# Kernel optimization log

Hardware: AMD Instinct MI355X
Metric: run time of the kernel (lower is better)

## Reference

```python
import jax, jax.numpy as jnp
import numpy as np

RES = 16            # voxel grid resolution (init arg res)
G = RES ** 3        # number of cells = 4096
REG_R = float(np.sqrt(3.0)) / RES  # sqrt(3)/s regularizer radius
B, C, RND, NPTS, H = 16, 64, 2, 16384, 256


def _grid_offsets():
    # util.meshgrid(res): integer grid coords, then ((grid+0.5)/res - 0.5).view(3,-1)
    r = jnp.arange(RES)
    gx, gy, gz = jnp.meshgrid(r, r, r, indexing='ij')
    grid = jnp.stack([gx, gy, gz], 0).reshape(3, -1).astype(jnp.float32)  # [3, G]
    return (grid + 0.5) / RES - 0.5


def _dens_sample(dens, n_points):
    # Deterministic largest-remainder allocation of n_points proportional to density.
    b = dens.shape[0]
    p = dens.reshape(b, -1)
    p = p / jnp.sum(p, axis=-1, keepdims=True)
    scaled = p * n_points                      # [b, G]
    base = jnp.floor(scaled)
    rem = (n_points - jnp.sum(base, axis=-1)).astype(jnp.int32)   # [b]
    frac = scaled - base
    ranks = jnp.argsort(jnp.argsort(-frac, axis=-1), axis=-1)      # rank by fractional part
    return base.astype(jnp.int32) + (ranks < rem[:, None]).astype(jnp.int32)  # [b, G]


def setup_inputs() -> dict:
    key = jax.random.key(0)
    ks = jax.random.split(key, 9)
    cin = C + RND
    f32 = jnp.float32
    return {
        'x': jax.random.normal(ks[0], (B, C, RES, RES, RES), f32),
        'dens': jax.random.uniform(ks[1], (B, RES, RES, RES), f32) + 1e-3,
        'noise': jax.random.uniform(ks[2], (B, RND, NPTS), f32),
        'W1': jax.random.normal(ks[3], (H, cin), f32) * np.float32(1.0 / np.sqrt(cin)),
        'b1': jnp.zeros((H,), f32),
        'W2': jax.random.normal(ks[4], (H, H), f32) * np.float32(1.0 / np.sqrt(H)),
        'b2': jnp.zeros((H,), f32),
        'W3': jax.random.normal(ks[5], (3, H), f32) * np.float32(1.0 / np.sqrt(H)),
        'b3': jnp.zeros((3,), f32),
        'n_points': NPTS,
    }


def reference(x, dens, noise, W1, b1, W2, b2, W3, b3, n_points):
    b, c = x.shape[0], x.shape[1]
    x_flat = x.reshape(b, c, -1)                        # [b, c, G]
    n = _dens_sample(dens, n_points)                    # [b, G] repeat counts, sums to n_points
    # Vectorized replacement for the nonzero()/cat loop: cell i appears n[i] times.
    cell_ids = jnp.arange(G)
    idx = jax.vmap(lambda ni: jnp.repeat(cell_ids, ni, total_repeat_length=n_points))(n)  # [b, n_points]
    x_ind = jnp.take_along_axis(x_flat, idx[:, None, :], axis=2)   # [b, c, n_points]
    o = _grid_offsets()                                 # [3, G]
    gen_off = jnp.transpose(o[:, idx], (1, 0, 2))       # [b, 3, n_points]
    rnd = noise * 2.0 - 1.0                             # uniform in [-1, 1)
    gen_inp = jnp.concatenate([x_ind, rnd], axis=1)     # [b, c+rnd, n_points]
    # pointwise conv1d MLP generator
    h = jax.nn.relu(jnp.einsum('oc,bcn->bon', W1, gen_inp) + b1[:, None])
    h = jax.nn.relu(jnp.einsum('oh,bhn->bon', W2, h) + b2[:, None])
    out = jnp.einsum('oh,bhn->bon', W3, h) + b3[:, None]            # [b, 3, n_points]
    norm = jnp.sqrt(jnp.sum(out * out, axis=1))                      # [b, n_points]
    reg = jnp.maximum(norm - REG_R, 0.0)
    return (out + gen_off, reg)
```

## Files before the change

kernel.cpp:

```cpp
#include <hip/hip_runtime.h>

typedef unsigned long long u64;
typedef _Float16 f16x8 __attribute__((ext_vector_type(8)));
typedef float    f32x4 __attribute__((ext_vector_type(4)));
typedef __fp16   fp16x2 __attribute__((ext_vector_type(2)));

#define G_    4096
#define NPTS  16384

union H8 { _Float16 h[8]; uint4 u; };
union PK2 { fp16x2 h[2]; uint2 u; };
union PK4 { fp16x2 h[4]; uint4 u; };

#define MFMA_(A_,B_,C_) __builtin_amdgcn_mfma_f32_16x16x32_f16((A_),(B_),(C_),0,0,0)


#define OFF_W1F 1048576
#define OFF_W2F 1097728
#define OFF_W3F 1228800
#define OFF_XT  1236992
#define WS_NEED (OFF_XT + 8388608)

__global__ __launch_bounds__(256) void kP(const float* __restrict__ dens,
                                          int* __restrict__ pc,
                                          const float* __restrict__ W1,
                                          const float* __restrict__ W2,
                                          const float* __restrict__ W3,
                                          const float* __restrict__ x,
                                          _Float16* __restrict__ w1f,
                                          _Float16* __restrict__ w2f,
                                          _Float16* __restrict__ w3f,
                                          _Float16* __restrict__ xT){
  __shared__ double sred[256];
  __shared__ u64  keys[4096];
  __shared__ int  nvs[4096];
  __shared__ int  binidx[4096];
  __shared__ int  hist[1024];
  __shared__ int  cab[1024];
  __shared__ int  scan[256];
  __shared__ float Sf;
  __shared__ int  remS, BstarS, needS, cntS;
  const int t = threadIdx.x;

  if (blockIdx.x >= 62){
    const int idx = blockIdx.x - 62;
    const int b = idx >> 4, blk = idx & 15;
    const int cell = blk*256 + t;
    const float* xb = x + ((size_t)b*64)*G_ + cell;
    _Float16* xo = xT + ((size_t)(b*G_ + cell))*64;
    #pragma unroll
    for (int c8 = 0; c8 < 8; ++c8){
      float a[8];
      #pragma unroll
      for (int j = 0; j < 8; ++j) a[j] = xb[(size_t)(c8*8 + j)*G_];
      PK4 v;
      v.h[0] = __builtin_amdgcn_cvt_pkrtz(a[0], a[1]);
      v.h[1] = __builtin_amdgcn_cvt_pkrtz(a[2], a[3]);
      v.h[2] = __builtin_amdgcn_cvt_pkrtz(a[4], a[5]);
      v.h[3] = __builtin_amdgcn_cvt_pkrtz(a[6], a[7]);
      *(uint4*)&xo[c8*8] = v.u;
    }
    return;
  }

  if (blockIdx.x >= 16){
    const int e = (blockIdx.x - 16)*256 + t;
    H8 v;
    if (e < 8192){
      const int RT = e >> 9, kt = (e >> 6) & 7, l = e & 63;
      const int m = RT*16 + (l & 15), k = kt*32 + ((l >> 4) << 3);
      #pragma unroll
      for (int j = 0; j < 8; ++j) v.h[j] = (_Float16)W2[m*256 + k + j];
      *(uint4*)&w2f[e*8] = v.u;
    } else if (e < 11264){
      const int e2 = e - 8192;
      const int RT = e2 / 192, r2 = e2 % 192, kt = r2 >> 6, l = r2 & 63;
      const int m = RT*16 + (l & 15), k = kt*32 + ((l >> 4) << 3);
      #pragma unroll
      for (int j = 0; j < 8; ++j) v.h[j] = (k + j < 66) ? (_Float16)W1[m*66 + k + j] : (_Float16)0.f;
      *(uint4*)&w1f[e2*8] = v.u;
    } else if (e < 11776){
      const int e3 = e - 11264;
      const int kt = e3 >> 6, l = e3 & 63;
      const int m = l & 15, k = kt*32 + ((l >> 4) << 3);
      #pragma unroll
      for (int j = 0; j < 8; ++j) v.h[j] = (m < 3) ? (_Float16)W3[m*256 + k + j] : (_Float16)0.f;
      *(uint4*)&w3f[e3*8] = v.u;
    }
    return;
  }

  const int b = blockIdx.x;
  const float* d = dens + b*G_;

  for (int j = t; j < 1024; j += 256) hist[j] = 0;
  if (t == 0) cntS = 0;

  double s = 0.0;
  for (int j = 0; j < 16; ++j) s += (double)d[t + 256*j];
  sred[t] = s; __syncthreads();
  for (int off = 128; off > 0; off >>= 1){
    if (t < off) sred[t] += sred[t + off];
    __syncthreads();
  }
  if (t == 0) Sf = (float)sred[0];
  __syncthreads();
  const float S = Sf;

  int bi[16]; int bs = 0;
  #pragma unroll
  for (int j = 0; j < 16; ++j){
    const int i = t + 256*j;
    const float p  = d[i] / S;
    const float sc = p * 16384.0f;
    const float fl = floorf(sc);
    const float fr = sc - fl;
    bi[j] = (int)fl; bs += bi[j];
    const unsigned fb = __float_as_uint(fr);
    keys[i] = ((u64)fb << 12) | (u64)(4095 - i);
    atomicAdd(&hist[fb >> 20], 1);
  }
  scan[t] = bs; __syncthreads();
  for (int off = 128; off > 0; off >>= 1){
    if (t < off) scan[t] += scan[t + off];
    __syncthreads();
  }
  if (t == 0) remS = 16384 - scan[0];
  __syncthreads();
  const int rem = remS;

  const int h0 = hist[4*t], h1 = hist[4*t+1], h2 = hist[4*t+2], h3 = hist[4*t+3];
  const int gs = h0 + h1 + h2 + h3;
  __syncthreads();
  scan[t] = gs; __syncthreads();
  for (int off = 1; off < 256; off <<= 1){
    const int v2 = (t + off < 256) ? scan[t + off] : 0;
    __syncthreads();
    scan[t] += v2;
    __syncthreads();
  }
  const int sAfter = scan[t] - gs;
  cab[4*t+3] = sAfter;
  cab[4*t+2] = sAfter + h3;
  cab[4*t+1] = sAfter + h3 + h2;
  cab[4*t+0] = sAfter + h3 + h2 + h1;
  if (t == 0){ BstarS = 0x7fffffff; needS = 0; }
  __syncthreads();
  if (rem > 0){
    const int ca[4] = {cab[4*t], cab[4*t+1], cab[4*t+2], cab[4*t+3]};
    const int hh[4] = {h0, h1, h2, h3};
    #pragma unroll
    for (int q = 0; q < 4; ++q)
      if (ca[q] < rem && rem <= ca[q] + hh[q]){ BstarS = 4*t + q; needS = rem - ca[q]; }
  }
  __syncthreads();
  const int Bstar = BstarS, need = needS;

  #pragma unroll
  for (int j = 0; j < 16; ++j){
    const int i = t + 256*j;
    const int bin = (int)(keys[i] >> 32);
    nvs[i] = bi[j] + ((bin > Bstar) ? 1 : 0);
    if (bin == Bstar){ const int pos = atomicAdd(&cntS, 1); binidx[pos] = i; }
  }
  __syncthreads();
  const int cnt = cntS;
  for (int p = t; p < cnt; p += 256){
    const u64 K = keys[binidx[p]];
    int r = 0;
    for (int q = 0; q < cnt; ++q) r += (keys[binidx[q]] > K) ? 1 : 0;
    if (r < need) nvs[binidx[p]] += 1;
  }
  __syncthreads();

  int loc[16]; int ls = 0;
  #pragma unroll
  for (int j = 0; j < 16; ++j){ loc[j] = nvs[t*16 + j]; ls += loc[j]; }
  __syncthreads();
  scan[t] = ls; __syncthreads();
  for (int off = 1; off < 256; off <<= 1){
    const int v2 = (t >= off) ? scan[t - off] : 0;
    __syncthreads();
    scan[t] += v2;
    __syncthreads();
  }
  int off0 = scan[t] - ls;
  int* o = pc + b*NPTS;
  #pragma unroll
  for (int j = 0; j < 16; ++j){
    const int c = t*16 + j;
    for (int r = 0; r < loc[j]; ++r) o[off0++] = c;
  }
}

template<bool USE_XT>
__global__ __launch_bounds__(256, 3) void kE(
    const float* __restrict__ x, const _Float16* __restrict__ xT,
    const float* __restrict__ noise,
    const _Float16* __restrict__ w1f, const _Float16* __restrict__ w2f,
    const _Float16* __restrict__ w3f,
    const float* __restrict__ b1, const float* __restrict__ b2, const float* __restrict__ b3,
    const int* __restrict__ pc, float* __restrict__ out)
{
  __shared__ _Float16 Hb[16384];
  __shared__ int cells[64];
  const int b = blockIdx.y, p0 = blockIdx.x*64, tid = threadIdx.x;
  const int w = tid >> 6, lane = tid & 63;

  if (tid < 64) cells[tid] = pc[b*NPTS + p0 + tid];

  {
    const int ct = tid >> 6, l2 = tid & 63;
    const int k2 = l2 >> 4, pt = ct*16 + (l2 & 15);
    PK4 v; v.u = make_uint4(0u, 0u, 0u, 0u);
    if (k2 == 0){
      const float n0 = noise[(b*2 + 0)*NPTS + p0 + pt]*2.f - 1.f;
      const float n1 = noise[(b*2 + 1)*NPTS + p0 + pt]*2.f - 1.f;
      v.h[0] = __builtin_amdgcn_cvt_pkrtz(n0, n1);
    }
    *(uint4*)&Hb[((2*4 + ct)*64 + l2)*8] = v.u;
  }

  #pragma unroll
  for (int i = 0; i < 2; ++i){
    const int e = tid + 256*i;
    const int pt = e >> 3, koct = e & 7;
    const int cell = pc[b*NPTS + p0 + pt];
    const int kt = koct >> 2, k2 = koct & 3;
    const int lane2 = (pt & 15) + k2*16, ct = pt >> 4;
    if (USE_XT){
      const uint4 v = *(const uint4*)&xT[((size_t)(b*G_ + cell))*64 + koct*8];
      *(uint4*)&Hb[((kt*4 + ct)*64 + lane2)*8] = v;
    } else {
      const float* xb = x + ((size_t)(b*64 + koct*8))*G_ + cell;
      float a[8];
      #pragma unroll
      for (int j = 0; j < 8; ++j) a[j] = xb[(size_t)j*G_];
      PK4 v;
      v.h[0] = __builtin_amdgcn_cvt_pkrtz(a[0], a[1]);
      v.h[1] = __builtin_amdgcn_cvt_pkrtz(a[2], a[3]);
      v.h[2] = __builtin_amdgcn_cvt_pkrtz(a[4], a[5]);
      v.h[3] = __builtin_amdgcn_cvt_pkrtz(a[6], a[7]);
      *(uint4*)&Hb[((kt*4 + ct)*64 + lane2)*8] = v.u;
    }
  }
  __syncthreads();

  f32x4 acc[4][4];
  const f32x4 zz = {0.f, 0.f, 0.f, 0.f};
  #pragma unroll
  for (int rt = 0; rt < 4; ++rt)
    #pragma unroll
    for (int ct = 0; ct < 4; ++ct) acc[rt][ct] = zz;

  const int wr = w*4;

  __builtin_amdgcn_s_setprio(1);
  #pragma unroll
  for (int kt = 0; kt < 3; ++kt){
    f16x8 B[4];
    #pragma unroll
    for (int ct = 0; ct < 4; ++ct) B[ct] = *(f16x8*)&Hb[((kt*4 + ct)*64 + lane)*8];
    #pragma unroll
    for (int rt = 0; rt < 4; ++rt){
      f16x8 A = *(const f16x8*)&w1f[(((wr + rt)*3 + kt)*64 + lane)*8];
      #pragma unroll
      for (int ct = 0; ct < 4; ++ct)
        acc[rt][ct] = MFMA_(A, B[ct], acc[rt][ct]);
    }
  }
  __builtin_amdgcn_s_setprio(0);
  __syncthreads();

  #pragma unroll
  for (int rt = 0; rt < 4; ++rt){
    const int row0 = w*64 + rt*16 + ((lane >> 4) << 2);
    const float4 bq = *(const float4*)&b1[row0];
    const int kt2 = row0 >> 5, c16 = (row0 >> 3) & 3, j0 = row0 & 7;
    const int lane2 = (lane & 15) + c16*16;
    #pragma unroll
    for (int ct = 0; ct < 4; ++ct){
      PK2 v;
      v.h[0] = __builtin_amdgcn_cvt_pkrtz(fmaxf(acc[rt][ct][0] + bq.x, 0.f),
                                          fmaxf(acc[rt][ct][1] + bq.y, 0.f));
      v.h[1] = __builtin_amdgcn_cvt_pkrtz(fmaxf(acc[rt][ct][2] + bq.z, 0.f),
                                          fmaxf(acc[rt][ct][3] + bq.w, 0.f));
      *(uint2*)&Hb[((kt2*4 + ct)*64 + lane2)*8 + j0] = v.u;
      acc[rt][ct] = zz;
    }
  }
  __syncthreads();

  __builtin_amdgcn_s_setprio(1);
  #pragma unroll 4
  for (int kt = 0; kt < 8; ++kt){
    f16x8 B[4];
    #pragma unroll
    for (int ct = 0; ct < 4; ++ct) B[ct] = *(f16x8*)&Hb[((kt*4 + ct)*64 + lane)*8];
    #pragma unroll
    for (int rt = 0; rt < 4; ++rt){
      f16x8 A = *(const f16x8*)&w2f[(((wr + rt)*8 + kt)*64 + lane)*8];
      #pragma unroll
      for (int ct = 0; ct < 4; ++ct)
        acc[rt][ct] = MFMA_(A, B[ct], acc[rt][ct]);
    }
  }
  __builtin_amdgcn_s_setprio(0);

  f16x8 W3v[8];
  #pragma unroll
  for (int kt = 0; kt < 8; ++kt) W3v[kt] = *(const f16x8*)&w3f[(kt*64 + lane)*8];
  __syncthreads();

  #pragma unroll
  for (int rt = 0; rt < 4; ++rt){
    const int row0 = w*64 + rt*16 + ((lane >> 4) << 2);
    const float4 bq = *(const float4*)&b2[row0];
    const int kt2 = row0 >> 5, c16 = (row0 >> 3) & 3, j0 = row0 & 7;
    const int lane2 = (lane & 15) + c16*16;
    #pragma unroll
    for (int ct = 0; ct < 4; ++ct){
      PK2 v;
      v.h[0] = __builtin_amdgcn_cvt_pkrtz(fmaxf(acc[rt][ct][0] + bq.x, 0.f),
                                          fmaxf(acc[rt][ct][1] + bq.y, 0.f));
      v.h[1] = __builtin_amdgcn_cvt_pkrtz(fmaxf(acc[rt][ct][2] + bq.z, 0.f),
                                          fmaxf(acc[rt][ct][3] + bq.w, 0.f));
      *(uint2*)&Hb[((kt2*4 + ct)*64 + lane2)*8 + j0] = v.u;
    }
  }
  __syncthreads();

  f32x4 a3 = zz;
  __builtin_amdgcn_s_setprio(1);
  #pragma unroll
  for (int kt = 0; kt < 8; ++kt){
    f16x8 B = *(f16x8*)&Hb[((kt*4 + w)*64 + lane)*8];
    a3 = MFMA_(W3v[kt], B, a3);
  }
  __builtin_amdgcn_s_setprio(0);
  if (lane < 16){
    const float ox = a3[0] + b3[0];
    const float oy = a3[1] + b3[1];
    const float oz = a3[2] + b3[2];
    const float nrm = sqrtf(ox*ox + oy*oy + oz*oz);
    const float rg_ = fmaxf(nrm - (float)0.10825317547305482, 0.f);
    const int pt = w*16 + lane;
    const int cell = cells[pt];
    const float fx = ((float)(cell >> 8)        + 0.5f) * 0.0625f - 0.5f;
    const float fy = ((float)((cell >> 4) & 15) + 0.5f) * 0.0625f - 0.5f;
    const float fz = ((float)(cell & 15)        + 0.5f) * 0.0625f - 0.5f;
    const int pidx = p0 + pt;
    out[b*49152 +          pidx] = ox + fx;
    out[b*49152 + 16384 +  pidx] = oy + fy;
    out[b*49152 + 32768 +  pidx] = oz + fz;
    out[786432  + b*16384 + pidx] = rg_;
  }
}

extern "C" void kernel_launch(void* const* d_in, const int* in_sizes, int n_in,
                              void* d_out, int out_size, void* d_ws, size_t ws_size,
                              hipStream_t stream){
  const float* x     = (const float*)d_in[0];
  const float* dens  = (const float*)d_in[1];
  const float* noise = (const float*)d_in[2];
  const float* W1    = (const float*)d_in[3];
  const float* b1    = (const float*)d_in[4];
  const float* W2    = (const float*)d_in[5];
  const float* b2    = (const float*)d_in[6];
  const float* W3    = (const float*)d_in[7];
  const float* b3    = (const float*)d_in[8];

  char* ws = (char*)d_ws;
  int*      pc   = (int*)(ws + 0);
  _Float16* w1f  = (_Float16*)(ws + OFF_W1F);
  _Float16* w2f  = (_Float16*)(ws + OFF_W2F);
  _Float16* w3f  = (_Float16*)(ws + OFF_W3F);
  _Float16* xT   = (_Float16*)(ws + OFF_XT);
  float*    out  = (float*)d_out;

  const bool use_xt = (ws_size >= (size_t)WS_NEED);
  const int  nprep  = use_xt ? 318 : 62;

  kP<<<dim3(nprep), dim3(256), 0, stream>>>(dens, pc, W1, W2, W3, x,
                                            w1f, w2f, w3f, xT);
  if (use_xt)
    kE<true ><<<dim3(256, 16), dim3(256), 0, stream>>>(x, xT, noise, w1f, w2f, w3f,
                                                       b1, b2, b3, pc, out);
  else
    kE<false><<<dim3(256, 16), dim3(256), 0, stream>>>(x, xT, noise, w1f, w2f, w3f,
                                                       b1, b2, b3, pc, out);
}
```

Baseline: 84.17 us.

## Make MLP kernel persistent over four point tiles with prefetched gather

Each block now processes four consecutive 64-point tiles in a loop instead of one, launching a quarter as many blocks. The next tile's cell indices, noise and gathered x features are loaded into registers during the current tile's layer-1 and layer-2 MFMA work, then written to a separate input LDS buffer. This hides gather latency behind compute and amortizes block setup, at the cost of fewer blocks (1024) for latency hiding and more LDS and register use.

```diff
diff --git a/kernel.cpp b/kernel.cpp
--- a/kernel.cpp
+++ b/kernel.cpp
@@ -11,6 +11,7 @@
 union H8 { _Float16 h[8]; uint4 u; };
 union PK2 { fp16x2 h[2]; uint2 u; };
 union PK4 { fp16x2 h[4]; uint4 u; };
+union PK1 { fp16x2 h; unsigned u; };
 
 #define MFMA_(A_,B_,C_) __builtin_amdgcn_mfma_f32_16x16x32_f16((A_),(B_),(C_),0,0,0)
 
@@ -202,158 +203,206 @@
     const float* __restrict__ b1, const float* __restrict__ b2, const float* __restrict__ b3,
     const int* __restrict__ pc, float* __restrict__ out)
 {
-  __shared__ _Float16 Hb[16384];
-  __shared__ int cells[64];
-  const int b = blockIdx.y, p0 = blockIdx.x*64, tid = threadIdx.x;
+  __shared__ _Float16 Hin[6144];
+  __shared__ _Float16 Bh[16384];
+  const int b = blockIdx.y, tid = threadIdx.x;
   const int w = tid >> 6, lane = tid & 63;
-
-  if (tid < 64) cells[tid] = pc[b*NPTS + p0 + tid];
-
+  const int base0 = b*NPTS + blockIdx.x*256;
+
+  const int ptA = tid >> 3, koct = tid & 7;
+  const int ptB = ptA + 32;
+  const int ktS = koct >> 2, k2 = koct & 3;
+  const int hinA = (((ktS*4 + (ptA >> 4))*64) + (ptA & 15) + k2*16)*8;
+  const int hinB = (((ktS*4 + (ptB >> 4))*64) + (ptB & 15) + k2*16)*8;
+  const int l2 = tid & 63;
+  const int npt = (tid >> 6)*16 + (tid & 15);
+  const int hinN = ((2*4 + (tid >> 6))*64 + l2)*8;
+
+  const f32x4 zz = {0.f, 0.f, 0.f, 0.f};
+  const int wr = w*4;
+
+  *(uint4*)&Hin[((2*4 + (tid >> 6))*64 + l2)*8] = make_uint4(0u,0u,0u,0u);
   {
-    const int ct = tid >> 6, l2 = tid & 63;
-    const int k2 = l2 >> 4, pt = ct*16 + (l2 & 15);
-    PK4 v; v.u = make_uint4(0u, 0u, 0u, 0u);
-    if (k2 == 0){
-      const float n0 = noise[(b*2 + 0)*NPTS + p0 + pt]*2.f - 1.f;
-      const float n1 = noise[(b*2 + 1)*NPTS + p0 + pt]*2.f - 1.f;
-      v.h[0] = __builtin_amdgcn_cvt_pkrtz(n0, n1);
-    }
-    *(uint4*)&Hb[((2*4 + ct)*64 + l2)*8] = v.u;
-  }
-
-  #pragma unroll
-  for (int i = 0; i < 2; ++i){
-    const int e = tid + 256*i;
-    const int pt = e >> 3, koct = e & 7;
-    const int cell = pc[b*NPTS + p0 + pt];
-    const int kt = koct >> 2, k2 = koct & 3;
-    const int lane2 = (pt & 15) + k2*16, ct = pt >> 4;
+    const int cA = pc[base0 + ptA];
+    const int cB = pc[base0 + ptB];
+    float n0 = 0.f, n1 = 0.f;
+    if (l2 < 16){
+      n0 = noise[(b*2 + 0)*NPTS + blockIdx.x*256 + npt]*2.f - 1.f;
+      n1 = noise[(b*2 + 1)*NPTS + blockIdx.x*256 + npt]*2.f - 1.f;
+    }
+    uint4 sA, sB;
     if (USE_XT){
-      const uint4 v = *(const uint4*)&xT[((size_t)(b*G_ + cell))*64 + koct*8];
-      *(uint4*)&Hb[((kt*4 + ct)*64 + lane2)*8] = v;
+      sA = *(const uint4*)&xT[((size_t)(b*G_ + cA))*64 + koct*8];
+      sB = *(const uint4*)&xT[((size_t)(b*G_ + cB))*64 + koct*8];
     } else {
-      const float* xb = x + ((size_t)(b*64 + koct*8))*G_ + cell;
-      float a[8];
-      #pragma unroll
-      for (int j = 0; j < 8; ++j) a[j] = xb[(size_t)j*G_];
-      PK4 v;
-      v.h[0] = __builtin_amdgcn_cvt_pkrtz(a[0], a[1]);
-      v.h[1] = __builtin_amdgcn_cvt_pkrtz(a[2], a[3]);
-      v.h[2] = __builtin_amdgcn_cvt_pkrtz(a[4], a[5]);
-      v.h[3] = __builtin_amdgcn_cvt_pkrtz(a[6], a[7]);
-      *(uint4*)&Hb[((kt*4 + ct)*64 + lane2)*8] = v.u;
-    }
-  }
-  __syncthreads();
-
-  f32x4 acc[4][4];
-  const f32x4 zz = {0.f, 0.f, 0.f, 0.f};
-  #pragma unroll
-  for (int rt = 0; rt < 4; ++rt)
-    #pragma unroll
-    for (int ct = 0; ct < 4; ++ct) acc[rt][ct] = zz;
-
-  const int wr = w*4;
-
-  __builtin_amdgcn_s_setprio(1);
-  #pragma unroll
-  for (int kt = 0; kt < 3; ++kt){
-    f16x8 B[4];
-    #pragma unroll
-    for (int ct = 0; ct < 4; ++ct) B[ct] = *(f16x8*)&Hb[((kt*4 + ct)*64 + lane)*8];
+      const float* xa = x + ((size_t)(b*64 + koct*8))*G_;
+      float a[8], c[8];
+      #pragma unroll
+      for (int j = 0; j < 8; ++j){ a[j] = xa[(size_t)j*G_ + cA]; c[j] = xa[(size_t)j*G_ + cB]; }
+      PK4 va, vb;
+      va.h[0] = __builtin_amdgcn_cvt_pkrtz(a[0],a[1]); va.h[1] = __builtin_amdgcn_cvt_pkrtz(a[2],a[3]);
+      va.h[2] = __builtin_amdgcn_cvt_pkrtz(a[4],a[5]); va.h[3] = __builtin_amdgcn_cvt_pkrtz(a[6],a[7]);
+      vb.h[0] = __builtin_amdgcn_cvt_pkrtz(c[0],c[1]); vb.h[1] = __builtin_amdgcn_cvt_pkrtz(c[2],c[3]);
+      vb.h[2] = __builtin_amdgcn_cvt_pkrtz(c[4],c[5]); vb.h[3] = __builtin_amdgcn_cvt_pkrtz(c[6],c[7]);
+      sA = va.u; sB = vb.u;
+    }
+    *(uint4*)&Hin[hinA] = sA;
+    *(uint4*)&Hin[hinB] = sB;
+    if (l2 < 16){
+      PK1 v; v.h = __builtin_amdgcn_cvt_pkrtz(n0, n1);
+      *(unsigned*)&Hin[hinN] = v.u;
+    }
+  }
+
+  #pragma unroll 1
+  for (int t = 0; t < 4; ++t){
+    const int p0  = blockIdx.x*256 + t*64;
+    const bool more = (t < 3);
+
+    int cA1 = 0, cB1 = 0; float m0 = 0.f, m1 = 0.f;
+    if (more){
+      cA1 = pc[b*NPTS + p0 + 64 + ptA];
+      cB1 = pc[b*NPTS + p0 + 64 + ptB];
+      if (l2 < 16){
+        m0 = noise[(b*2 + 0)*NPTS + p0 + 64 + npt]*2.f - 1.f;
+        m1 = noise[(b*2 + 1)*NPTS + p0 + 64 + npt]*2.f - 1.f;
+      }
+    }
+    const int cellO = pc[b*NPTS + p0 + w*16 + (lane & 15)];
+
+    f32x4 acc[4][4];
+    #pragma unroll
+    for (int rt = 0; rt < 4; ++rt)
+      #pragma unroll
+      for (int ct = 0; ct < 4; ++ct) acc[rt][ct] = zz;
+
+    __syncthreads();
+
+    __builtin_amdgcn_s_setprio(1);
+    #pragma unroll
+    for (int kt = 0; kt < 3; ++kt){
+      f16x8 B[4];
+      #pragma unroll
+      for (int ct = 0; ct < 4; ++ct) B[ct] = *(f16x8*)&Hin[((kt*4 + ct)*64 + lane)*8];
+      #pragma unroll
+      for (int rt = 0; rt < 4; ++rt){
+        f16x8 A = *(const f16x8*)&w1f[(((wr + rt)*3 + kt)*64 + lane)*8];
+        #pragma unroll
+        for (int ct = 0; ct < 4; ++ct)
+          acc[rt][ct] = MFMA_(A, B[ct], acc[rt][ct]);
+      }
+    }
+    __builtin_amdgcn_s_setprio(0);
+
+    uint4 sA1 = make_uint4(0u,0u,0u,0u), sB1 = sA1;
+    if (more){
+      if (USE_XT){
+        sA1 = *(const uint4*)&xT[((size_t)(b*G_ + cA1))*64 + koct*8];
+        sB1 = *(const uint4*)&xT[((size_t)(b*G_ + cB1))*64 + koct*8];
+      } else {
+        const float* xa = x + ((size_t)(b*64 + koct*8))*G_;
+        float a[8], c[8];
+        #pragma unroll
+        for (int j = 0; j < 8; ++j){ a[j] = xa[(size_t)j*G_ + cA1]; c[j] = xa[(size_t)j*G_ + cB1]; }
+        PK4 va, vb;
+        va.h[0] = __builtin_amdgcn_cvt_pkrtz(a[0],a[1]); va.h[1] = __builtin_amdgcn_cvt_pkrtz(a[2],a[3]);
+        va.h[2] = __builtin_amdgcn_cvt_pkrtz(a[4],a[5]); va.h[3] = __builtin_amdgcn_cvt_pkrtz(a[6],a[7]);
+        vb.h[0] = __builtin_amdgcn_cvt_pkrtz(c[0],c[1]); vb.h[1] = __builtin_amdgcn_cvt_pkrtz(c[2],c[3]);
+        vb.h[2] = __builtin_amdgcn_cvt_pkrtz(c[4],c[5]); vb.h[3] = __builtin_amdgcn_cvt_pkrtz(c[6],c[7]);
+        sA1 = va.u; sB1 = vb.u;
+      }
+    }
+
     #pragma unroll
     for (int rt = 0; rt < 4; ++rt){
-      f16x8 A = *(const f16x8*)&w1f[(((wr + rt)*3 + kt)*64 + lane)*8];
-      #pragma unroll
-      for (int ct = 0; ct < 4; ++ct)
-        acc[rt][ct] = MFMA_(A, B[ct], acc[rt][ct]);
-    }
-  }
-  __builtin_amdgcn_s_setprio(0);
-  __syncthreads();
-
-  #pragma unroll
-  for (int rt = 0; rt < 4; ++rt){
-    const int row0 = w*64 + rt*16 + ((lane >> 4) << 2);
-    const float4 bq = *(const float4*)&b1[row0];
-    const int kt2 = row0 >> 5, c16 = (row0 >> 3) & 3, j0 = row0 & 7;
-    const int lane2 = (lane & 15) + c16*16;
-    #pragma unroll
-    for (int ct = 0; ct < 4; ++ct){
-      PK2 v;
-      v.h[0] = __builtin_amdgcn_cvt_pkrtz(fmaxf(acc[rt][ct][0] + bq.x, 0.f),
-                                          fmaxf(acc[rt][ct][1] + bq.y, 0.f));
-      v.h[1] = __builtin_amdgcn_cvt_pkrtz(fmaxf(acc[rt][ct][2] + bq.z, 0.f),
-                                          fmaxf(acc[rt][ct][3] + bq.w, 0.f));
-      *(uint2*)&Hb[((kt2*4 + ct)*64 + lane2)*8 + j0] = v.u;
-      acc[rt][ct] = zz;
-    }
-  }
-  __syncthreads();
-
-  __builtin_amdgcn_s_setprio(1);
-  #pragma unroll 4
-  for (int kt = 0; kt < 8; ++kt){
-    f16x8 B[4];
-    #pragma unroll
-    for (int ct = 0; ct < 4; ++ct) B[ct] = *(f16x8*)&Hb[((kt*4 + ct)*64 + lane)*8];
+      const int row0 = w*64 + rt*16 + ((lane >> 4) << 2);
+      const float4 bq = *(const float4*)&b1[row0];
+      const int kt2 = row0 >> 5, c16 = (row0 >> 3) & 3, j0 = row0 & 7;
+      const int lane2 = (lane & 15) + c16*16;
+      #pragma unroll
+      for (int ct = 0; ct < 4; ++ct){
+        PK2 v;
+        v.h[0] = __builtin_amdgcn_cvt_pkrtz(fmaxf(acc[rt][ct][0] + bq.x, 0.f),
+                                            fmaxf(acc[rt][ct][1] + bq.y, 0.f));
+        v.h[1] = __builtin_amdgcn_cvt_pkrtz(fmaxf(acc[rt][ct][2] + bq.z, 0.f),
+                                            fmaxf(acc[rt][ct][3] + bq.w, 0.f));
+        *(uint2*)&Bh[((kt2*4 + ct)*64 + lane2)*8 + j0] = v.u;
+        acc[rt][ct] = zz;
+      }
+    }
+    __syncthreads();
+
+    __builtin_amdgcn_s_setprio(1);
+    #pragma unroll 4
+    for (int kt = 0; kt < 8; ++kt){
+      f16x8 B[4];
+      #pragma unroll
+      for (int ct = 0; ct < 4; ++ct) B[ct] = *(f16x8*)&Bh[((kt*4 + ct)*64 + lane)*8];
+      #pragma unroll
+      for (int rt = 0; rt < 4; ++rt){
+        f16x8 A = *(const f16x8*)&w2f[(((wr + rt)*8 + kt)*64 + lane)*8];
+        #pragma unroll
+        for (int ct = 0; ct < 4; ++ct)
+          acc[rt][ct] = MFMA_(A, B[ct], acc[rt][ct]);
+      }
+    }
+    __builtin_amdgcn_s_setprio(0);
+
+    if (more){
+      *(uint4*)&Hin[hinA] = sA1;
+      *(uint4*)&Hin[hinB] = sB1;
+      if (l2 < 16){
+        PK1 v; v.h = __builtin_amdgcn_cvt_pkrtz(m0, m1);
+        *(unsigned*)&Hin[hinN] = v.u;
+      }
+    }
+
+    f16x8 W3v[8];
+    #pragma unroll
+    for (int kt = 0; kt < 8; ++kt) W3v[kt] = *(const f16x8*)&w3f[(kt*64 + lane)*8];
+    __syncthreads();
+
     #pragma unroll
     for (int rt = 0; rt < 4; ++rt){
-      f16x8 A = *(const f16x8*)&w2f[(((wr + rt)*8 + kt)*64 + lane)*8];
-      #pragma unroll
-      for (int ct = 0; ct < 4; ++ct)
-        acc[rt][ct] = MFMA_(A, B[ct], acc[rt][ct]);
-    }
-  }
-  __builtin_amdgcn_s_setprio(0);
-
-  f16x8 W3v[8];
-  #pragma unroll
-  for (int kt = 0; kt < 8; ++kt) W3v[kt] = *(const f16x8*)&w3f[(kt*64 + lane)*8];
-  __syncthreads();
-
-  #pragma unroll
-  for (int rt = 0; rt < 4; ++rt){
-    const int row0 = w*64 + rt*16 + ((lane >> 4) << 2);
-    const float4 bq = *(const float4*)&b2[row0];
-    const int kt2 = row0 >> 5, c16 = (row0 >> 3) & 3, j0 = row0 & 7;
-    const int lane2 = (lane & 15) + c16*16;
-    #pragma unroll
-    for (int ct = 0; ct < 4; ++ct){
-      PK2 v;
-      v.h[0] = __builtin_amdgcn_cvt_pkrtz(fmaxf(acc[rt][ct][0] + bq.x, 0.f),
-                                          fmaxf(acc[rt][ct][1] + bq.y, 0.f));
-      v.h[1] = __builtin_amdgcn_cvt_pkrtz(fmaxf(acc[rt][ct][2] + bq.z, 0.f),
-                                          fmaxf(acc[rt][ct][3] + bq.w, 0.f));
-      *(uint2*)&Hb[((kt2*4 + ct)*64 + lane2)*8 + j0] = v.u;
-    }
-  }
-  __syncthreads();
-
-  f32x4 a3 = zz;
-  __builtin_amdgcn_s_setprio(1);
-  #pragma unroll
-  for (int kt = 0; kt < 8; ++kt){
-    f16x8 B = *(f16x8*)&Hb[((kt*4 + w)*64 + lane)*8];
-    a3 = MFMA_(W3v[kt], B, a3);
-  }
-  __builtin_amdgcn_s_setprio(0);
-  if (lane < 16){
-    const float ox = a3[0] + b3[0];
-    const float oy = a3[1] + b3[1];
-    const float oz = a3[2] + b3[2];
-    const float nrm = sqrtf(ox*ox + oy*oy + oz*oz);
-    const float rg_ = fmaxf(nrm - (float)0.10825317547305482, 0.f);
-    const int pt = w*16 + lane;
-    const int cell = cells[pt];
-    const float fx = ((float)(cell >> 8)        + 0.5f) * 0.0625f - 0.5f;
-    const float fy = ((float)((cell >> 4) & 15) + 0.5f) * 0.0625f - 0.5f;
-    const float fz = ((float)(cell & 15)        + 0.5f) * 0.0625f - 0.5f;
-    const int pidx = p0 + pt;
-    out[b*49152 +          pidx] = ox + fx;
-    out[b*49152 + 16384 +  pidx] = oy + fy;
-    out[b*49152 + 32768 +  pidx] = oz + fz;
-    out[786432  + b*16384 + pidx] = rg_;
+      const int row0 = w*64 + rt*16 + ((lane >> 4) << 2);
+      const float4 bq = *(const float4*)&b2[row0];
+      const int kt2 = row0 >> 5, c16 = (row0 >> 3) & 3, j0 = row0 & 7;
+      const int lane2 = (lane & 15) + c16*16;
+      #pragma unroll
+      for (int ct = 0; ct < 4; ++ct){
+        PK2 v;
+        v.h[0] = __builtin_amdgcn_cvt_pkrtz(fmaxf(acc[rt][ct][0] + bq.x, 0.f),
+                                            fmaxf(acc[rt][ct][1] + bq.y, 0.f));
+        v.h[1] = __builtin_amdgcn_cvt_pkrtz(fmaxf(acc[rt][ct][2] + bq.z, 0.f),
+                                            fmaxf(acc[rt][ct][3] + bq.w, 0.f));
+        *(uint2*)&Bh[((kt2*4 + ct)*64 + lane2)*8 + j0] = v.u;
+      }
+    }
+    __syncthreads();
+
+    f32x4 a3 = zz;
+    __builtin_amdgcn_s_setprio(1);
+    #pragma unroll
+    for (int kt = 0; kt < 8; ++kt){
+      f16x8 B = *(f16x8*)&Bh[((kt*4 + w)*64 + lane)*8];
+      a3 = MFMA_(W3v[kt], B, a3);
+    }
+    __builtin_amdgcn_s_setprio(0);
+    if (lane < 16){
+      const float ox = a3[0] + b3[0];
+      const float oy = a3[1] + b3[1];
+      const float oz = a3[2] + b3[2];
+      const float nrm = sqrtf(ox*ox + oy*oy + oz*oz);
+      const float rg_ = fmaxf(nrm - (float)0.10825317547305482, 0.f);
+      const float fx = ((float)(cellO >> 8)        + 0.5f) * 0.0625f - 0.5f;
+      const float fy = ((float)((cellO >> 4) & 15) + 0.5f) * 0.0625f - 0.5f;
+      const float fz = ((float)(cellO & 15)        + 0.5f) * 0.0625f - 0.5f;
+      const int pidx = p0 + w*16 + lane;
+      out[b*49152 +          pidx] = ox + fx;
+      out[b*49152 + 16384 +  pidx] = oy + fy;
+      out[b*49152 + 32768 +  pidx] = oz + fz;
+      out[786432  + b*16384 + pidx] = rg_;
+    }
   }
 }
 
@@ -384,9 +433,9 @@
   kP<<<dim3(nprep), dim3(256), 0, stream>>>(dens, pc, W1, W2, W3, x,
                                             w1f, w2f, w3f, xT);
   if (use_xt)
-    kE<true ><<<dim3(256, 16), dim3(256), 0, stream>>>(x, xT, noise, w1f, w2f, w3f,
-                                                       b1, b2, b3, pc, out);
+    kE<true ><<<dim3(64, 16), dim3(256), 0, stream>>>(x, xT, noise, w1f, w2f, w3f,
+                                                      b1, b2, b3, pc, out);
   else
-    kE<false><<<dim3(256, 16), dim3(256), 0, stream>>>(x, xT, noise, w1f, w2f, w3f,
-                                                       b1, b2, b3, pc, out);
+    kE<false><<<dim3(64, 16), dim3(256), 0, stream>>>(x, xT, noise, w1f, w2f, w3f,
+                                                      b1, b2, b3, pc, out);
 }
```

Result: slower. 249.2 us (+196.0%).
